# Kernel tuning notes

Measured on AMD Instinct MI355X. Metric: run time of the kernel, lower is better.

The kernel has to match this reference:

```python
import jax, jax.numpy as jnp
import numpy as np

B, N, E = 2, 2048, 1024
H = 16
NE = 16                                  # num experts
TOPN = 2
CAP = max(4, int(N * 1.25 / NE))         # expert capacity = 160 (train, cf=1.25)
HFF = int(E * 4 * 2 / 3)                 # 2730, Expert_alt hidden
EPS = 1e-9
BLOCK = 64                               # spatial block size for block-causal mask


def setup_inputs():
    key = jax.random.key(0)
    ks = jax.random.split(key, 16)
    def nrm(k, shape, s=0.02):
        return jax.random.normal(k, shape, dtype=jnp.float32) * s
    # block-causal mask (tril over time blocks, repeat_interleave spatially); True = masked
    blk = np.tril(np.ones((N // BLOCK, N // BLOCK)))
    blk = np.repeat(np.repeat(blk, BLOCK, axis=0), BLOCK, axis=1)
    attn_mask = jnp.asarray(~blk.astype(bool))
    return dict(
        x=jax.random.normal(ks[0], (B, N, E), jnp.float32),
        attn_mask=attn_mask,
        in_proj_w=nrm(ks[1], (3 * E, E)),
        in_proj_b=jnp.zeros((3 * E,), jnp.float32),
        out_proj_w=nrm(ks[2], (E, E)),
        out_proj_b=jnp.zeros((E,), jnp.float32),
        rms_gamma=jnp.ones((E,), jnp.float32),
        gate_w=nrm(ks[3], (NE, E)),
        ln_g=jnp.ones((NE, E), jnp.float32),
        ln_b=jnp.zeros((NE, E), jnp.float32),
        w1=nrm(ks[4], (NE, HFF, E)),
        b1=jnp.zeros((NE, HFF), jnp.float32),
        w2=nrm(ks[5], (NE, E, HFF)),
        b2=jnp.zeros((NE, E), jnp.float32),
        route_unif=jax.random.uniform(ks[6], (TOPN, B, N), jnp.float32),
    )


def _layernorm(t, g, b, eps=1e-5):
    mu = t.mean(-1, keepdims=True)
    var = ((t - mu) ** 2).mean(-1, keepdims=True)
    return (t - mu) * jax.lax.rsqrt(var + eps) * g + b


def _forward(x, attn_mask, in_proj_w, in_proj_b, out_proj_w, out_proj_b,
             rms_gamma, gate_w, ln_g, ln_b, w1, b1, w2, b2, route_unif):
    dh = E // H
    # ---- multi-head self-attention (torch nn.MultiheadAttention math) ----
    qkv = x @ in_proj_w.T + in_proj_b                       # (B,N,3E)
    q, k, v = jnp.split(qkv, 3, axis=-1)
    to_heads = lambda t: t.reshape(B, N, H, dh).transpose(0, 2, 1, 3)
    q, k, v = to_heads(q), to_heads(k), to_heads(v)
    scores = jnp.einsum('bhqd,bhkd->bhqk', q, k) / jnp.sqrt(jnp.float32(dh))
    scores = jnp.where(attn_mask[None, None], -jnp.inf, scores)
    attn = jax.nn.softmax(scores, axis=-1)
    o = jnp.einsum('bhqk,bhkd->bhqd', attn, v).transpose(0, 2, 1, 3).reshape(B, N, E)
    o = o @ out_proj_w.T + out_proj_b
    y = o + x                                               # residual around MHA

    # ---- SparseMoEBlock: RMSNorm prenorm -> MoE -> residual ----
    residual = y
    nrm = y / jnp.clip(jnp.linalg.norm(y, axis=-1, keepdims=True), 1e-12)
    moe_in = nrm * jnp.sqrt(jnp.float32(E)) * rms_gamma

    # ---- top-2 gating (st-moe TopNGating, training mode) ----
    logits = moe_in @ gate_w.T                              # (B,N,NE)
    raw_gates = jax.nn.softmax(logits, axis=-1)
    gates_v, gate_idx = jax.lax.top_k(raw_gates, TOPN)      # (B,N,2)
    gates = jnp.moveaxis(gates_v, -1, 0)                    # (2,B,N)
    gate_idx = jnp.moveaxis(gate_idx, -1, 0)
    one_hot_idx = jax.nn.one_hot(gate_idx, NE, dtype=jnp.float32)  # (2,B,N,NE)
    mask = one_hot_idx
    mask_1 = mask[0]
    denom = jnp.clip(gates.sum(0, keepdims=True), EPS)
    gates = gates / denom
    threshold = jnp.array([EPS, 0.2], jnp.float32)[:, None, None]
    should_route = route_unif < gates / jnp.clip(threshold, EPS)
    should_route = should_route.at[0].set(True)             # always route to top-1
    mask = mask * should_route[..., None].astype(jnp.float32)
    mask_cumsum = jnp.cumsum(mask, axis=-2) - mask          # exclusive cumsum over N

    positions, masks_k = [], []
    prev = jnp.zeros((B, 1, NE), jnp.float32)
    capf = jnp.float32(CAP)
    for n_ in range(TOPN):
        pos = (mask_cumsum[n_] + prev) * mask[n_]           # (B,N,NE)
        mk = mask[n_] * (pos < capf).astype(jnp.float32)    # drop over-capacity
        prev = prev + mk.sum(axis=-2, keepdims=True)
        positions.append(pos.sum(-1))                       # (B,N)
        masks_k.append(mk)
    positions = jnp.stack(positions)                        # (2,B,N)
    mask = jnp.stack(masks_k)
    mask_flat = mask.sum(-1)                                # (2,B,N)
    gates = gates * mask_flat

    pos_oh = jax.nn.one_hot(positions.astype(jnp.int32), CAP, dtype=jnp.float32)  # (2,B,N,CAP)
    combine = jnp.einsum('kbn,kbn,kbne,kbnc->bnec', gates, mask_flat, one_hot_idx, pos_oh)
    dispatch_hard = (combine > 0).astype(jnp.float32)
    dispatch = dispatch_hard + combine - jax.lax.stop_gradient(combine)  # straight-through

    # ---- aux losses ----
    density_1 = mask_1.mean(-2)                             # (B,NE)
    density_proxy = raw_gates.mean(-2)
    balance_loss = (density_proxy * density_1).mean() * jnp.float32(NE ** 2)
    router_z_loss = jnp.mean(jax.nn.logsumexp(logits, axis=-1) ** 2)

    # ---- dispatch -> experts -> combine ----
    expert_inputs = jnp.einsum('bnd,bnec->ebcd', moe_in, dispatch)  # (NE,B,CAP,E)

    def expert_fn(g, bl, W1, B1, W2, B2, xin):
        h = _layernorm(xin, g, bl)
        h = h @ W1.T + B1
        h = jnp.where(h >= 0, h, 0.01 * h)                  # LeakyReLU(0.01)
        return h @ W2.T + B2

    expert_out = jax.vmap(expert_fn)(ln_g, ln_b, w1, b1, w2, b2, expert_inputs)
    moe_out = jnp.einsum('bnec,ebcd->bnd', combine, expert_out)

    out = moe_out + residual
    total_aux = balance_loss * 0.01 + router_z_loss * 0.001
    return out, total_aux, balance_loss, router_z_loss


def reference(x, attn_mask, in_proj_w, in_proj_b, out_proj_w, out_proj_b,
              rms_gamma, gate_w, ln_g, ln_b, w1, b1, w2, b2, route_unif):
    return _forward(x, attn_mask, in_proj_w, in_proj_b, out_proj_w, out_proj_b,
                    rms_gamma, gate_w, ln_g, ln_b, w1, b1, w2, b2, route_unif)
```

## Files before the change

kernel.cpp:

```cpp
#include <hip/hip_runtime.h>
#include <hip/hip_bf16.h>
#include <cstdint>

#define NSEQ  2048
#define BSZ   2
#define NTOK  4096
#define EDIM  1024
#define NEXP  16
#define CAPC  160
#define HFF_R 2730
#define HFF_P 2752

typedef __bf16 bf16_t;
typedef __bf16 bf16x8 __attribute__((ext_vector_type(8)));
typedef __bf16 bf16x4 __attribute__((ext_vector_type(4)));
typedef float  f32x4  __attribute__((ext_vector_type(4)));
typedef unsigned int uint32;

__device__ inline bf16x8 zero8() {
    bf16x8 v;
#pragma unroll
    for (int i = 0; i < 8; i++) v[i] = (bf16_t)0.f;
    return v;
}
__device__ inline bf16x8 pack8(float4 a, float4 b) {
    bf16x8 v;
    v[0]=(bf16_t)a.x; v[1]=(bf16_t)a.y; v[2]=(bf16_t)a.z; v[3]=(bf16_t)a.w;
    v[4]=(bf16_t)b.x; v[5]=(bf16_t)b.y; v[6]=(bf16_t)b.z; v[7]=(bf16_t)b.w;
    return v;
}
struct hl_t { bf16_t h, l; };
__device__ inline hl_t split1(float f) {
    hl_t r;
    r.h = (bf16_t)f;
    r.l = (bf16_t)(f - (float)r.h);
    return r;
}

__global__ __launch_bounds__(256) void split_kernel(const float* __restrict__ src,
                                                    bf16_t* __restrict__ hi,
                                                    bf16_t* __restrict__ lo, int n)
{
    int i = (blockIdx.x * 256 + threadIdx.x) * 4;
    if (i >= n) return;
    float4 v = *(const float4*)(src + i);
    hl_t a = split1(v.x), b = split1(v.y), c = split1(v.z), d = split1(v.w);
    bf16x4 h, l;
    h[0] = a.h; h[1] = b.h; h[2] = c.h; h[3] = d.h;
    l[0] = a.l; l[1] = b.l; l[2] = c.l; l[3] = d.l;
    *(bf16x4*)(hi + i) = h;
    *(bf16x4*)(lo + i) = l;
}

template <int EPI, int C_SPLIT>
__global__ __launch_bounds__(256) void gemm_ps(
    const bf16_t* __restrict__ Ah_, const bf16_t* __restrict__ Al_,
    const bf16_t* __restrict__ Bh_, const bf16_t* __restrict__ Bl_,
    const float* __restrict__ bias, const float* __restrict__ resid,
    bf16_t* __restrict__ Chi, bf16_t* __restrict__ Clo, float* __restrict__ Cf,
    int M, int N, int K, int scale_cut, float scale_val)
{
    __shared__ __align__(16) bf16_t Ah[128 * 40], Al[128 * 40];
    __shared__ __align__(16) bf16_t Bh[128 * 40], Bl[128 * 40];
    const int t = threadIdx.x;
    const int m0 = blockIdx.y * 128, n0 = blockIdx.x * 128;
    const int lane = t & 63, l15 = lane & 15, lg = lane >> 4;
    const int wid = t >> 6, wm = wid >> 1, wn = wid & 1;
    const int srow = t >> 1, skc = (t & 1) * 16;

    f32x4 acc[4][4];
    const f32x4 zf = {0.f, 0.f, 0.f, 0.f};
#pragma unroll
    for (int i = 0; i < 4; i++)
#pragma unroll
        for (int j = 0; j < 4; j++) acc[i][j] = zf;

    bf16x8 sah0, sah1, sal0, sal1, sbh0, sbh1, sbl0, sbl1;
    auto LOADAB = [&](int k0) {
        long aoff = (long)(m0 + srow) * K + k0 + skc;
        sah0 = *(const bf16x8*)(Ah_ + aoff); sah1 = *(const bf16x8*)(Ah_ + aoff + 8);
        sal0 = *(const bf16x8*)(Al_ + aoff); sal1 = *(const bf16x8*)(Al_ + aoff + 8);
        long boff = (long)(n0 + srow) * K + k0 + skc;
        sbh0 = *(const bf16x8*)(Bh_ + boff); sbh1 = *(const bf16x8*)(Bh_ + boff + 8);
        sbl0 = *(const bf16x8*)(Bl_ + boff); sbl1 = *(const bf16x8*)(Bl_ + boff + 8);
    };
    auto WRITEAB = [&]() {
        *(bf16x8*)&Ah[srow * 40 + skc] = sah0; *(bf16x8*)&Ah[srow * 40 + skc + 8] = sah1;
        *(bf16x8*)&Al[srow * 40 + skc] = sal0; *(bf16x8*)&Al[srow * 40 + skc + 8] = sal1;
        *(bf16x8*)&Bh[srow * 40 + skc] = sbh0; *(bf16x8*)&Bh[srow * 40 + skc + 8] = sbh1;
        *(bf16x8*)&Bl[srow * 40 + skc] = sbl0; *(bf16x8*)&Bl[srow * 40 + skc + 8] = sbl1;
    };

    LOADAB(0);
    for (int k0 = 0; k0 < K; k0 += 32) {
        WRITEAB();
        __syncthreads();
        if (k0 + 32 < K) LOADAB(k0 + 32);
        bf16x8 amh[4], aml[4], bnh[4], bnl[4];
#pragma unroll
        for (int i = 0; i < 4; i++) {
            int base = (wm * 64 + i * 16 + l15) * 40 + lg * 8;
            amh[i] = *(const bf16x8*)&Ah[base];
            aml[i] = *(const bf16x8*)&Al[base];
        }
#pragma unroll
        for (int j = 0; j < 4; j++) {
            int base = (wn * 64 + j * 16 + l15) * 40 + lg * 8;
            bnh[j] = *(const bf16x8*)&Bh[base];
            bnl[j] = *(const bf16x8*)&Bl[base];
        }
        __builtin_amdgcn_s_setprio(1);
#pragma unroll
        for (int i = 0; i < 4; i++)
#pragma unroll
            for (int j = 0; j < 4; j++) {
                acc[i][j] = __builtin_amdgcn_mfma_f32_16x16x32_bf16(amh[i], bnh[j], acc[i][j], 0, 0, 0);
                acc[i][j] = __builtin_amdgcn_mfma_f32_16x16x32_bf16(amh[i], bnl[j], acc[i][j], 0, 0, 0);
                acc[i][j] = __builtin_amdgcn_mfma_f32_16x16x32_bf16(aml[i], bnh[j], acc[i][j], 0, 0, 0);
            }
        __builtin_amdgcn_s_setprio(0);
        __syncthreads();
    }

#pragma unroll
    for (int i = 0; i < 4; i++) {
        int mgb = m0 + wm * 64 + i * 16 + lg * 4;
#pragma unroll
        for (int j = 0; j < 4; j++) {
            int ng = n0 + wn * 64 + j * 16 + l15;
            float bval = bias[ng];
#pragma unroll
            for (int r = 0; r < 4; r++) {
                int mg = mgb + r;
                float val = acc[i][j][r] + bval;
                if (scale_cut > 0 && ng < scale_cut) val *= scale_val;
                if (EPI == 2) val += resid[(long)mg * N + ng];
                long idx = (long)mg * N + ng;
                if (C_SPLIT) {
                    bf16_t hi = (bf16_t)val;
                    Chi[idx] = hi;
                    Clo[idx] = (bf16_t)(val - (float)hi);
                } else {
                    Cf[idx] = val;
                }
            }
        }
    }
}

template <int EPI, int C_BF16>
__global__ __launch_bounds__(256) void gemm_ffn(
    const bf16_t* __restrict__ Av, const float* __restrict__ Bw,
    const float* __restrict__ bias, void* __restrict__ Cv,
    int N, int Nwr, int KA, int KB,
    long sAe, long sBe, long sBiasE, long sCe, int ldc)
{
    __shared__ __align__(16) bf16_t Alds[320 * 72];
    __shared__ __align__(16) bf16_t Blds[64 * 72];
    const int id = blockIdx.x;
    const int e = id & 15, nt = id >> 4;
    const int n0 = nt * 64;
    const int t = threadIdx.x;
    const int lane = t & 63, l15 = lane & 15, lg = lane >> 4;
    const int wid = t >> 6, wm = wid >> 1, wn = wid & 1;
    const int srow = t >> 2, scol = (t & 3) * 16;

    f32x4 acc[10][2];
    const f32x4 zf = {0.f, 0.f, 0.f, 0.f};
#pragma unroll
    for (int i = 0; i < 10; i++)
#pragma unroll
        for (int j = 0; j < 2; j++) acc[i][j] = zf;

    bf16x8 sa[5][2];
    float4 sb0, sb1, sb2, sb3;
    const float4 zf4 = {0.f, 0.f, 0.f, 0.f};
    auto LOADA = [&](int k0) {
        const bf16_t* abase = Av + (long)e * sAe + k0 + scol;
#pragma unroll
        for (int p = 0; p < 5; p++) {
            const bf16_t* ap = abase + (long)(srow + 64 * p) * KA;
            sa[p][0] = *(const bf16x8*)ap;
            sa[p][1] = *(const bf16x8*)(ap + 8);
        }
    };
    auto LOADB = [&](int k0) {
        int ng = n0 + srow;
        if (ng < N) {
            const float* bp = Bw + (long)e * sBe + (long)ng * KB + k0 + scol;
            if (k0 + 64 <= KB) {
                sb0 = *(const float4*)bp;       sb1 = *(const float4*)(bp + 4);
                sb2 = *(const float4*)(bp + 8); sb3 = *(const float4*)(bp + 12);
            } else {
                float v[16];
#pragma unroll
                for (int i = 0; i < 16; i++) {
                    int kk = k0 + scol + i;
                    v[i] = (kk < KB) ? bp[i] : 0.f;
                }
                sb0 = *(float4*)&v[0];  sb1 = *(float4*)&v[4];
                sb2 = *(float4*)&v[8];  sb3 = *(float4*)&v[12];
            }
        } else {
            sb0 = zf4; sb1 = zf4; sb2 = zf4; sb3 = zf4;
        }
    };
    auto WRITEAB = [&]() {
#pragma unroll
        for (int p = 0; p < 5; p++) {
            *(bf16x8*)&Alds[(srow + 64 * p) * 72 + scol]     = sa[p][0];
            *(bf16x8*)&Alds[(srow + 64 * p) * 72 + scol + 8] = sa[p][1];
        }
        *(bf16x8*)&Blds[srow * 72 + scol]     = pack8(sb0, sb1);
        *(bf16x8*)&Blds[srow * 72 + scol + 8] = pack8(sb2, sb3);
    };

    LOADA(0); LOADB(0);
    for (int k0 = 0; k0 < KA; k0 += 64) {
        WRITEAB();
        __syncthreads();
        if (k0 + 64 < KA) { LOADA(k0 + 64); LOADB(k0 + 64); }
#pragma unroll
        for (int ks = 0; ks < 2; ks++) {
            bf16x8 bn[2];
#pragma unroll
            for (int j = 0; j < 2; j++)
                bn[j] = *(const bf16x8*)&Blds[(wn * 32 + j * 16 + l15) * 72 + ks * 32 + lg * 8];
            bf16x8 am[10];
#pragma unroll
            for (int i = 0; i < 10; i++)
                am[i] = *(const bf16x8*)&Alds[(wm * 160 + i * 16 + l15) * 72 + ks * 32 + lg * 8];
            __builtin_amdgcn_s_setprio(1);
#pragma unroll
            for (int i = 0; i < 10; i++)
#pragma unroll
                for (int j = 0; j < 2; j++)
                    acc[i][j] = __builtin_amdgcn_mfma_f32_16x16x32_bf16(am[i], bn[j], acc[i][j], 0, 0, 0);
            __builtin_amdgcn_s_setprio(0);
        }
        __syncthreads();
    }

    const float* biasp = bias + (long)e * sBiasE;
#pragma unroll
    for (int i = 0; i < 10; i++) {
        int mgb = wm * 160 + i * 16 + lg * 4;
#pragma unroll
        for (int j = 0; j < 2; j++) {
            int ng = n0 + wn * 32 + j * 16 + l15;
            if (ng < Nwr) {
                float bval = (ng < N) ? biasp[ng] : 0.f;
#pragma unroll
                for (int r = 0; r < 4; r++) {
                    int mg = mgb + r;
                    float val = acc[i][j][r] + bval;
                    if (EPI == 1) val = (val >= 0.f) ? val : 0.01f * val;
                    if (ng >= N) val = 0.f;
                    long cidx = (long)e * sCe + (long)mg * ldc + ng;
                    if (C_BF16) ((bf16_t*)Cv)[cidx] = (bf16_t)val;
                    else        ((float*)Cv)[cidx] = val;
                }
            }
        }
    }
}

__global__ __launch_bounds__(256) void attn_split(const bf16_t* __restrict__ qh,
                                                  const bf16_t* __restrict__ ql,
                                                  bf16_t* __restrict__ oh,
                                                  bf16_t* __restrict__ ol)
{
    __shared__ __align__(16) bf16_t KhS[64 * 72], KlS[64 * 72];
    __shared__ __align__(16) bf16_t VhS[64 * 72], VlS[64 * 72];
    __shared__ __align__(16) bf16_t PhS[4][2][16 * 72], PlS[4][2][16 * 72];

    const int id = blockIdx.x;
    const int x  = id & 7;
    const int s  = id >> 3;
    const int b  = s >> 5;
    const int s5 = s & 31;
    const int qraw = s5 & 15;
    const int h  = x + 8 * (s5 >> 4);
    const int qt = b ? (15 - qraw) : qraw;
    const int nkb = 2 * qt + 2;

    const int t = threadIdx.x, wid = t >> 6, lane = t & 63, l15 = lane & 15, lg = lane >> 4;
    const int krow = t >> 2, kdc = (t & 3) * 16;
    const int vk = t & 63, vdg = (t >> 6) * 16;
    const long kvb = (long)(b * NSEQ) * 3072 + 1024 + h * 64;
    const f32x4 zf = {0.f, 0.f, 0.f, 0.f};

    const long qo0 = (long)(b * NSEQ + qt * 128 + wid * 16 + l15) * 3072 + h * 64 + lg * 8;
    const long qo1 = qo0 + (long)64 * 3072;
    bf16x8 q0h0 = *(const bf16x8*)(qh + qo0), q0h1 = *(const bf16x8*)(qh + qo0 + 32);
    bf16x8 q0l0 = *(const bf16x8*)(ql + qo0), q0l1 = *(const bf16x8*)(ql + qo0 + 32);
    bf16x8 q1h0 = *(const bf16x8*)(qh + qo1), q1h1 = *(const bf16x8*)(qh + qo1 + 32);
    bf16x8 q1l0 = *(const bf16x8*)(ql + qo1), q1l1 = *(const bf16x8*)(ql + qo1 + 32);

    f32x4 O0[4], O1[4];
    float m0r[4], l0r[4], m1r[4], l1r[4];
#pragma unroll
    for (int r = 0; r < 4; r++) {
        O0[r] = zf; O1[r] = zf;
        m0r[r] = -1e30f; l0r[r] = 0.f; m1r[r] = -1e30f; l1r[r] = 0.f;
    }

    bf16x8 skh0, skh1, skl0, skl1, svh0, svh1, svl0, svl1;
    auto LOADKV = [&](int kb) {
        long ko = kvb + (long)(kb * 64 + krow) * 3072 + kdc;
        skh0 = *(const bf16x8*)(qh + ko); skh1 = *(const bf16x8*)(qh + ko + 8);
        skl0 = *(const bf16x8*)(ql + ko); skl1 = *(const bf16x8*)(ql + ko + 8);
        long vo = kvb + 1024 + (long)(kb * 64 + vk) * 3072 + vdg;
        svh0 = *(const bf16x8*)(qh + vo); svh1 = *(const bf16x8*)(qh + vo + 8);
        svl0 = *(const bf16x8*)(ql + vo); svl1 = *(const bf16x8*)(ql + vo + 8);
    };
    auto WRITEKV = [&]() {
        *(bf16x8*)&KhS[krow * 72 + kdc]     = skh0;
        *(bf16x8*)&KhS[krow * 72 + kdc + 8] = skh1;
        *(bf16x8*)&KlS[krow * 72 + kdc]     = skl0;
        *(bf16x8*)&KlS[krow * 72 + kdc + 8] = skl1;
#pragma unroll
        for (int i = 0; i < 8; i++) {
            VhS[(vdg + i) * 72 + vk]     = svh0[i];
            VhS[(vdg + 8 + i) * 72 + vk] = svh1[i];
            VlS[(vdg + i) * 72 + vk]     = svl0[i];
            VlS[(vdg + 8 + i) * 72 + vk] = svl1[i];
        }
    };

    LOADKV(0);
    for (int kb = 0; kb < nkb; kb++) {
        __syncthreads();
        WRITEKV();
        __syncthreads();
        if (kb + 1 < nkb) LOADKV(kb + 1);
        const bool g0a = (kb < nkb - 1);
        f32x4 s0[4], s1[4];
        __builtin_amdgcn_s_setprio(1);
#pragma unroll
        for (int ks = 0; ks < 4; ks++) {
            int base = (ks * 16 + l15) * 72 + lg * 8;
            bf16x8 kh0 = *(const bf16x8*)&KhS[base];
            bf16x8 kh1 = *(const bf16x8*)&KhS[base + 32];
            bf16x8 kl0 = *(const bf16x8*)&KlS[base];
            bf16x8 kl1 = *(const bf16x8*)&KlS[base + 32];
            f32x4 a = zf;
            a = __builtin_amdgcn_mfma_f32_16x16x32_bf16(q1h0, kh0, a, 0, 0, 0);
            a = __builtin_amdgcn_mfma_f32_16x16x32_bf16(q1h1, kh1, a, 0, 0, 0);
            a = __builtin_amdgcn_mfma_f32_16x16x32_bf16(q1h0, kl0, a, 0, 0, 0);
            a = __builtin_amdgcn_mfma_f32_16x16x32_bf16(q1h1, kl1, a, 0, 0, 0);
            a = __builtin_amdgcn_mfma_f32_16x16x32_bf16(q1l0, kh0, a, 0, 0, 0);
            a = __builtin_amdgcn_mfma_f32_16x16x32_bf16(q1l1, kh1, a, 0, 0, 0);
            s1[ks] = a;
            f32x4 c = zf;
            if (g0a) {
                c = __builtin_amdgcn_mfma_f32_16x16x32_bf16(q0h0, kh0, c, 0, 0, 0);
                c = __builtin_amdgcn_mfma_f32_16x16x32_bf16(q0h1, kh1, c, 0, 0, 0);
                c = __builtin_amdgcn_mfma_f32_16x16x32_bf16(q0h0, kl0, c, 0, 0, 0);
                c = __builtin_amdgcn_mfma_f32_16x16x32_bf16(q0h1, kl1, c, 0, 0, 0);
                c = __builtin_amdgcn_mfma_f32_16x16x32_bf16(q0l0, kh0, c, 0, 0, 0);
                c = __builtin_amdgcn_mfma_f32_16x16x32_bf16(q0l1, kh1, c, 0, 0, 0);
            }
            s0[ks] = c;
        }
        __builtin_amdgcn_s_setprio(0);
        {
            float alpha[4];
#pragma unroll
            for (int r = 0; r < 4; r++) {
                float mt = fmaxf(fmaxf(s1[0][r], s1[1][r]), fmaxf(s1[2][r], s1[3][r]));
#pragma unroll
                for (int m = 1; m < 16; m <<= 1) mt = fmaxf(mt, __shfl_xor(mt, m));
                float mn = fmaxf(m1r[r], mt);
                alpha[r] = __expf(m1r[r] - mn);
                m1r[r] = mn;
            }
            float ladd[4] = {0.f, 0.f, 0.f, 0.f};
#pragma unroll
            for (int ks = 0; ks < 4; ks++)
#pragma unroll
                for (int r = 0; r < 4; r++) {
                    float p = __expf(s1[ks][r] - m1r[r]);
                    s1[ks][r] = p;
                    ladd[r] += p;
                }
#pragma unroll
            for (int r = 0; r < 4; r++) {
#pragma unroll
                for (int m = 1; m < 16; m <<= 1) ladd[r] += __shfl_xor(ladd[r], m);
                l1r[r] = l1r[r] * alpha[r] + ladd[r];
            }
#pragma unroll
            for (int sb = 0; sb < 4; sb++)
#pragma unroll
                for (int r = 0; r < 4; r++) O1[sb][r] *= alpha[r];
            bf16_t* pwh = &PhS[wid][1][0];
            bf16_t* pwl = &PlS[wid][1][0];
#pragma unroll
            for (int ks = 0; ks < 4; ks++)
#pragma unroll
                for (int r = 0; r < 4; r++) {
                    hl_t pv = split1(s1[ks][r]);
                    pwh[(lg * 4 + r) * 72 + ks * 16 + l15] = pv.h;
                    pwl[(lg * 4 + r) * 72 + ks * 16 + l15] = pv.l;
                }
        }
        if (g0a) {
            float alpha[4];
#pragma unroll
            for (int r = 0; r < 4; r++) {
                float mt = fmaxf(fmaxf(s0[0][r], s0[1][r]), fmaxf(s0[2][r], s0[3][r]));
#pragma unroll
                for (int m = 1; m < 16; m <<= 1) mt = fmaxf(mt, __shfl_xor(mt, m));
                float mn = fmaxf(m0r[r], mt);
                alpha[r] = __expf(m0r[r] - mn);
                m0r[r] = mn;
            }
            float ladd[4] = {0.f, 0.f, 0.f, 0.f};
#pragma unroll
            for (int ks = 0; ks < 4; ks++)
#pragma unroll
                for (int r = 0; r < 4; r++) {
                    float p = __expf(s0[ks][r] - m0r[r]);
                    s0[ks][r] = p;
                    ladd[r] += p;
                }
#pragma unroll
            for (int r = 0; r < 4; r++) {
#pragma unroll
                for (int m = 1; m < 16; m <<= 1) ladd[r] += __shfl_xor(ladd[r], m);
                l0r[r] = l0r[r] * alpha[r] + ladd[r];
            }
#pragma unroll
            for (int sb = 0; sb < 4; sb++)
#pragma unroll
                for (int r = 0; r < 4; r++) O0[sb][r] *= alpha[r];
            bf16_t* pwh = &PhS[wid][0][0];
            bf16_t* pwl = &PlS[wid][0][0];
#pragma unroll
            for (int ks = 0; ks < 4; ks++)
#pragma unroll
                for (int r = 0; r < 4; r++) {
                    hl_t pv = split1(s0[ks][r]);
                    pwh[(lg * 4 + r) * 72 + ks * 16 + l15] = pv.h;
                    pwl[(lg * 4 + r) * 72 + ks * 16 + l15] = pv.l;
                }
        }
        __builtin_amdgcn_s_setprio(1);
#pragma unroll
        for (int kst = 0; kst < 2; kst++) {
            bf16x8 pf1h = *(const bf16x8*)&PhS[wid][1][l15 * 72 + kst * 32 + lg * 8];
            bf16x8 pf1l = *(const bf16x8*)&PlS[wid][1][l15 * 72 + kst * 32 + lg * 8];
            bf16x8 pf0h, pf0l;
            if (g0a) {
                pf0h = *(const bf16x8*)&PhS[wid][0][l15 * 72 + kst * 32 + lg * 8];
                pf0l = *(const bf16x8*)&PlS[wid][0][l15 * 72 + kst * 32 + lg * 8];
            }
#pragma unroll
            for (int sb = 0; sb < 4; sb++) {
                int base = (sb * 16 + l15) * 72 + kst * 32 + lg * 8;
                bf16x8 vfh = *(const bf16x8*)&VhS[base];
                bf16x8 vfl = *(const bf16x8*)&VlS[base];
                O1[sb] = __builtin_amdgcn_mfma_f32_16x16x32_bf16(pf1h, vfh, O1[sb], 0, 0, 0);
                O1[sb] = __builtin_amdgcn_mfma_f32_16x16x32_bf16(pf1h, vfl, O1[sb], 0, 0, 0);
                O1[sb] = __builtin_amdgcn_mfma_f32_16x16x32_bf16(pf1l, vfh, O1[sb], 0, 0, 0);
                if (g0a) {
                    O0[sb] = __builtin_amdgcn_mfma_f32_16x16x32_bf16(pf0h, vfh, O0[sb], 0, 0, 0);
                    O0[sb] = __builtin_amdgcn_mfma_f32_16x16x32_bf16(pf0h, vfl, O0[sb], 0, 0, 0);
                    O0[sb] = __builtin_amdgcn_mfma_f32_16x16x32_bf16(pf0l, vfh, O0[sb], 0, 0, 0);
                }
            }
        }
        __builtin_amdgcn_s_setprio(0);
    }
#pragma unroll
    for (int sb = 0; sb < 4; sb++)
#pragma unroll
        for (int r = 0; r < 4; r++) {
            int qg0 = qt * 128 + wid * 16 + lg * 4 + r;
            int col = h * 64 + sb * 16 + l15;
            long i0 = (long)(b * NSEQ + qg0) * 1024 + col;
            long i1 = (long)(b * NSEQ + qg0 + 64) * 1024 + col;
            hl_t v0 = split1(O0[sb][r] / l0r[r]);
            hl_t v1 = split1(O1[sb][r] / l1r[r]);
            oh[i0] = v0.h; ol[i0] = v0.l;
            oh[i1] = v1.h; ol[i1] = v1.l;
        }
}

__global__ __launch_bounds__(256) void rmsnorm_kernel(const float* __restrict__ y,
                                                      const float* __restrict__ gamma,
                                                      float* __restrict__ moe)
{
    long base = (long)blockIdx.x * 1024;
    float4 v = ((const float4*)(y + base))[threadIdx.x];
    float ss = v.x * v.x + v.y * v.y + v.z * v.z + v.w * v.w;
#pragma unroll
    for (int m = 32; m; m >>= 1) ss += __shfl_xor(ss, m);
    __shared__ float ls[4];
    if ((threadIdx.x & 63) == 0) ls[threadIdx.x >> 6] = ss;
    __syncthreads();
    float tot = ls[0] + ls[1] + ls[2] + ls[3];
    float sc = 32.0f / fmaxf(sqrtf(tot), 1e-12f);
    float4 g = ((const float4*)gamma)[threadIdx.x];
    float4 ov;
    ov.x = v.x * sc * g.x; ov.y = v.y * sc * g.y; ov.z = v.z * sc * g.z; ov.w = v.w * sc * g.w;
    ((float4*)(moe + base))[threadIdx.x] = ov;
}

__global__ __launch_bounds__(256) void gating_kernel(
    const float* __restrict__ moe, const float* __restrict__ gw,
    const float* __restrict__ runif, uint32* __restrict__ tokpack,
    float* __restrict__ tokg, float* __restrict__ acc)
{
    const int wid = threadIdx.x >> 6, lane = threadIdx.x & 63;
    const int tk = blockIdx.x * 4 + wid;
    const int b = tk >> 11, n = tk & 2047;
    float xv[16];
    const float4* xr4 = (const float4*)(moe + (long)tk * 1024 + lane * 16);
#pragma unroll
    for (int i = 0; i < 4; i++) {
        float4 v = xr4[i];
        xv[4 * i] = v.x; xv[4 * i + 1] = v.y; xv[4 * i + 2] = v.z; xv[4 * i + 3] = v.w;
    }
    float logit[16];
#pragma unroll
    for (int e = 0; e < 16; e++) {
        const float4* wr4 = (const float4*)(gw + e * 1024 + lane * 16);
        float p = 0.f;
#pragma unroll
        for (int i = 0; i < 4; i++) {
            float4 w = wr4[i];
            p = fmaf(xv[4 * i], w.x, p);     p = fmaf(xv[4 * i + 1], w.y, p);
            p = fmaf(xv[4 * i + 2], w.z, p); p = fmaf(xv[4 * i + 3], w.w, p);
        }
#pragma unroll
        for (int m = 1; m < 64; m <<= 1) p += __shfl_xor(p, m);
        logit[e] = p;
    }
    int e0 = 0; float t0 = logit[0];
#pragma unroll
    for (int e = 1; e < 16; e++) if (logit[e] > t0) { t0 = logit[e]; e0 = e; }
    int e1 = (e0 == 0) ? 1 : 0; float t1 = logit[e1];
#pragma unroll
    for (int e = 0; e < 16; e++) if (e != e0 && logit[e] > t1) { t1 = logit[e]; e1 = e; }
    float g0n = 1.f / (1.f + __expf(t1 - t0));
    float g1n = 1.f / (1.f + __expf(t0 - t1));
    int sr1 = (runif[(long)(BSZ + b) * NSEQ + n] < g1n / 0.2f) ? 1 : 0;
    float mx = t0, sum = 0.f, raw[16];
#pragma unroll
    for (int e = 0; e < 16; e++) { raw[e] = __expf(logit[e] - mx); sum += raw[e]; }
    float inv = 1.f / sum;
    float lse = mx + __logf(sum);
    if (lane == 0) {
        tokpack[tk] = (uint32)e0 | ((uint32)e1 << 4) | ((uint32)sr1 << 8);
        tokg[2 * tk] = g0n; tokg[2 * tk + 1] = g1n;
        atomicAdd(&acc[32 + b * 16 + e0], 1.0f);
        atomicAdd(&acc[64], lse * lse);
    }
    if (lane < 16) atomicAdd(&acc[b * 16 + lane], raw[lane] * inv);
}

__global__ __launch_bounds__(512) void scan_kernel(const uint32* __restrict__ tokpack,
                                                   uint32* __restrict__ r0,
                                                   uint32* __restrict__ r1,
                                                   int* __restrict__ prev)
{
    const int b = blockIdx.x, t = threadIdx.x;
    const int wv = t >> 6, lane = t & 63;
    uint32 toks[4];
    *(uint4*)toks = ((const uint4*)(tokpack + b * NSEQ))[t];

    uint32 c0[8], c1[8];
#pragma unroll
    for (int j = 0; j < 8; j++) { c0[j] = 0u; c1[j] = 0u; }
#pragma unroll
    for (int i = 0; i < 4; i++) {
        uint32 p = toks[i];
        uint32 e0 = p & 15, e1 = (p >> 4) & 15, sr1 = (p >> 8) & 1;
        uint32 inc0 = 1u << ((e0 & 1) * 16);
        uint32 inc1 = sr1 << ((e1 & 1) * 16);
#pragma unroll
        for (int j = 0; j < 8; j++) {
            c0[j] += ((e0 >> 1) == (uint32)j) ? inc0 : 0u;
            c1[j] += ((e1 >> 1) == (uint32)j) ? inc1 : 0u;
        }
    }
    uint32 i0[8], i1[8];
#pragma unroll
    for (int j = 0; j < 8; j++) { i0[j] = c0[j]; i1[j] = c1[j]; }
#pragma unroll
    for (int off = 1; off < 64; off <<= 1) {
#pragma unroll
        for (int j = 0; j < 8; j++) {
            uint32 u0 = __shfl_up(i0[j], off);
            uint32 u1 = __shfl_up(i1[j], off);
            if (lane >= off) { i0[j] += u0; i1[j] += u1; }
        }
    }
    __shared__ uint32 wsum0[8][8], wsum1[8][8];
    if (lane == 63) {
#pragma unroll
        for (int j = 0; j < 8; j++) { wsum0[wv][j] = i0[j]; wsum1[wv][j] = i1[j]; }
    }
    __syncthreads();
    uint32 b0[8], b1[8];
#pragma unroll
    for (int j = 0; j < 8; j++) {
        uint32 s0 = 0u, s1 = 0u;
#pragma unroll
        for (int w = 0; w < 8; w++) {
            s0 += (w < wv) ? wsum0[w][j] : 0u;
            s1 += (w < wv) ? wsum1[w][j] : 0u;
        }
        b0[j] = s0 + i0[j] - c0[j];
        b1[j] = s1 + i1[j] - c1[j];
    }
    if (t == 0) {
#pragma unroll
        for (int j = 0; j < 8; j++) {
            uint32 tot = 0u;
#pragma unroll
            for (int w = 0; w < 8; w++) tot += wsum0[w][j];
            int tlo = (int)(tot & 0xffffu), thi = (int)(tot >> 16);
            prev[b * 16 + 2 * j]     = tlo < CAPC ? tlo : CAPC;
            prev[b * 16 + 2 * j + 1] = thi < CAPC ? thi : CAPC;
        }
    }
    uint32* rr0 = r0 + b * NSEQ + t * 4;
    uint32* rr1 = r1 + b * NSEQ + t * 4;
#pragma unroll
    for (int i = 0; i < 4; i++) {
        uint32 p = toks[i];
        uint32 e0 = p & 15, e1 = (p >> 4) & 15, sr1 = (p >> 8) & 1;
        uint32 sh0 = (e0 & 1) * 16, sh1 = (e1 & 1) * 16;
        uint32 w0 = 0u, w1 = 0u;
#pragma unroll
        for (int j = 0; j < 8; j++) {
            w0 += ((e0 >> 1) == (uint32)j) ? b0[j] : 0u;
            w1 += ((e1 >> 1) == (uint32)j) ? b1[j] : 0u;
        }
        uint32 s0 = (w0 >> sh0) & 0xffffu;
        uint32 s1v = (w1 >> sh1) & 0xffffu;
        uint32 kept = (s0 < CAPC) ? 1u : 0u;
        rr0[i] = e0 | (kept << 4) | (s0 << 5);
        rr1[i] = e1 | (sr1 << 4) | (s1v << 5);
        uint32 inc0 = 1u << sh0;
        uint32 inc1 = sr1 << sh1;
#pragma unroll
        for (int j = 0; j < 8; j++) {
            b0[j] += ((e0 >> 1) == (uint32)j) ? inc0 : 0u;
            b1[j] += ((e1 >> 1) == (uint32)j) ? inc1 : 0u;
        }
    }
}

__global__ __launch_bounds__(256) void gather_kernel(
    const float* __restrict__ moe, const uint32* __restrict__ r0,
    const uint32* __restrict__ r1, const int* __restrict__ prev,
    float* __restrict__ ein)
{
    int tk = blockIdx.x, b = tk >> 11;
    float4 v = ((const float4*)(moe + (long)tk * 1024))[threadIdx.x];
    uint32 a = r0[tk];
    if ((a >> 4) & 1) {
        long row = ((long)(a & 15) * 2 + b) * CAPC + (int)(a >> 5);
        ((float4*)(ein + row * 1024))[threadIdx.x] = v;
    }
    uint32 c = r1[tk];
    {
        int e = c & 15, sr1 = (c >> 4) & 1;
        int slot = (int)(c >> 5) + prev[b * 16 + e];
        if (sr1 && slot < CAPC) {
            long row = ((long)e * 2 + b) * CAPC + slot;
            ((float4*)(ein + row * 1024))[threadIdx.x] = v;
        }
    }
}

__global__ __launch_bounds__(256) void expert_ln_kernel(
    const float* __restrict__ ein, const float* __restrict__ g,
    const float* __restrict__ bb, bf16_t* __restrict__ eout)
{
    int row = blockIdx.x, e = row / (BSZ * CAPC);
    long base = (long)row * 1024;
    float4 v = ((const float4*)(ein + base))[threadIdx.x];
    float s = v.x + v.y + v.z + v.w;
    float ss = v.x * v.x + v.y * v.y + v.z * v.z + v.w * v.w;
#pragma unroll
    for (int m = 32; m; m >>= 1) { s += __shfl_xor(s, m); ss += __shfl_xor(ss, m); }
    __shared__ float l1[4], l2[4];
    if ((threadIdx.x & 63) == 0) { l1[threadIdx.x >> 6] = s; l2[threadIdx.x >> 6] = ss; }
    __syncthreads();
    float st = l1[0] + l1[1] + l1[2] + l1[3];
    float sst = l2[0] + l2[1] + l2[2] + l2[3];
    float mu = st * (1.f / 1024.f);
    float var = sst * (1.f / 1024.f) - mu * mu;
    float rstd = rsqrtf(var + 1e-5f);
    int d = threadIdx.x * 4;
    float4 gg = *(const float4*)(g + e * 1024 + d);
    float4 bv = *(const float4*)(bb + e * 1024 + d);
    bf16x4 ov;
    ov[0] = (bf16_t)((v.x - mu) * rstd * gg.x + bv.x);
    ov[1] = (bf16_t)((v.y - mu) * rstd * gg.y + bv.y);
    ov[2] = (bf16_t)((v.z - mu) * rstd * gg.z + bv.z);
    ov[3] = (bf16_t)((v.w - mu) * rstd * gg.w + bv.w);
    *(bf16x4*)(eout + base + d) = ov;
}

__global__ __launch_bounds__(256) void combine_kernel(
    const float* __restrict__ y, const float* __restrict__ eout,
    const uint32* __restrict__ r0, const uint32* __restrict__ r1,
    const float* __restrict__ tokg, const int* __restrict__ prev,
    float* __restrict__ out)
{
    int tk = blockIdx.x, b = tk >> 11;
    uint32 a = r0[tk], c = r1[tk];
    int k0f = (a >> 4) & 1;
    float w0 = k0f ? tokg[2 * tk] : 0.f;
    long row0 = ((long)(a & 15) * 2 + b) * CAPC + (int)(a >> 5);
    int e1 = c & 15;
    int slot1 = (int)(c >> 5) + prev[b * 16 + e1];
    int k1f = (((c >> 4) & 1) && slot1 < CAPC) ? 1 : 0;
    float w1 = k1f ? tokg[2 * tk + 1] : 0.f;
    long row1 = ((long)e1 * 2 + b) * CAPC + slot1;
    int i = threadIdx.x;
    float4 vy = ((const float4*)(y + (long)tk * 1024))[i];
    float4 a0 = {0.f, 0.f, 0.f, 0.f}, a1 = {0.f, 0.f, 0.f, 0.f};
    if (k0f) a0 = ((const float4*)(eout + row0 * 1024))[i];
    if (k1f) a1 = ((const float4*)(eout + row1 * 1024))[i];
    float4 ov;
    ov.x = vy.x + w0 * a0.x + w1 * a1.x;
    ov.y = vy.y + w0 * a0.y + w1 * a1.y;
    ov.z = vy.z + w0 * a0.z + w1 * a1.z;
    ov.w = vy.w + w0 * a0.w + w1 * a1.w;
    ((float4*)(out + (long)tk * 1024))[i] = ov;
}

__global__ void zero_acc_kernel(float* acc)
{
    if (threadIdx.x < 65) acc[threadIdx.x] = 0.f;
}

__global__ void finalize_kernel(const float* __restrict__ acc, float* __restrict__ tail)
{
    int t = threadIdx.x;
    float v = (t < 32) ? acc[t] * acc[32 + t] : 0.f;
#pragma unroll
    for (int m = 1; m < 64; m <<= 1) v += __shfl_xor(v, m);
    if (t == 0) {
        float bal = v * (8.0f / (2048.f * 2048.f));
        float z = acc[64] / 4096.f;
        tail[0] = 0.01f * bal + 0.001f * z;
        tail[1] = bal;
        tail[2] = z;
    }
}

extern "C" void kernel_launch(void* const* d_in, const int* in_sizes, int n_in,
                              void* d_out, int out_size, void* d_ws, size_t ws_size,
                              hipStream_t stream)
{
    (void)in_sizes; (void)n_in; (void)out_size; (void)ws_size;
    const float* x     = (const float*)d_in[0];
    const float* in_w  = (const float*)d_in[2];
    const float* in_b  = (const float*)d_in[3];
    const float* out_w = (const float*)d_in[4];
    const float* out_b = (const float*)d_in[5];
    const float* rg    = (const float*)d_in[6];
    const float* gw    = (const float*)d_in[7];
    const float* lng   = (const float*)d_in[8];
    const float* lnb   = (const float*)d_in[9];
    const float* w1    = (const float*)d_in[10];
    const float* b1    = (const float*)d_in[11];
    const float* w2    = (const float*)d_in[12];
    const float* b2    = (const float*)d_in[13];
    const float* runif = (const float*)d_in[14];
    float* out = (float*)d_out;

    size_t off = 0;
    char* wsb = (char*)d_ws;
    auto take = [&](size_t bytes) -> char* {
        char* p = wsb + off;
        off += (bytes + 255) & ~(size_t)255;
        return p;
    };
    bf16_t* qkvh = (bf16_t*)take((size_t)NTOK * 3072 * 2);
    bf16_t* qkvl = (bf16_t*)take((size_t)NTOK * 3072 * 2);
    bf16_t* oh   = (bf16_t*)take((size_t)NTOK * 1024 * 2);
    bf16_t* ol   = (bf16_t*)take((size_t)NTOK * 1024 * 2);
    float*  ybuf = (float*)take((size_t)NTOK * 1024 * 4);
    float*  moe  = (float*)take((size_t)NTOK * 1024 * 4);
    bf16_t* eln  = (bf16_t*)take((size_t)NEXP * BSZ * CAPC * 1024 * 2);
    bf16_t* hbuf = (bf16_t*)take((size_t)NEXP * BSZ * CAPC * HFF_P * 2);
    bf16_t* owh  = (bf16_t*)take((size_t)1024 * 1024 * 2);
    bf16_t* owl  = (bf16_t*)take((size_t)1024 * 1024 * 2);
    uint32* tokpack = (uint32*)take(NTOK * 4);
    float*  tokg = (float*)take(NTOK * 8);
    uint32* r0   = (uint32*)take(NTOK * 4);
    uint32* r1   = (uint32*)take(NTOK * 4);
    int*    prev = (int*)take(128);
    float*  acc  = (float*)take(1024);
    float*  ein   = (float*)qkvl;
    float*  eoutv = (float*)qkvh;
    bf16_t* xh    = eln;
    bf16_t* xl    = xh + (size_t)NTOK * 1024;
    bf16_t* iwh   = xl + (size_t)NTOK * 1024;
    bf16_t* iwl   = iwh + (size_t)3072 * 1024;

    zero_acc_kernel<<<1, 128, 0, stream>>>(acc);

    split_kernel<<<dim3(NTOK * 1024 / 1024), 256, 0, stream>>>(x, xh, xl, NTOK * 1024);
    split_kernel<<<dim3(3072 * 1024 / 1024), 256, 0, stream>>>(in_w, iwh, iwl, 3072 * 1024);
    split_kernel<<<dim3(1024 * 1024 / 1024), 256, 0, stream>>>(out_w, owh, owl, 1024 * 1024);

    gemm_ps<0, 1><<<dim3(24, 32), 256, 0, stream>>>(
        xh, xl, iwh, iwl, in_b, nullptr, qkvh, qkvl, nullptr,
        NTOK, 3072, 1024, 1024, 0.125f);

    attn_split<<<dim3(512), 256, 0, stream>>>(qkvh, qkvl, oh, ol);

    gemm_ps<2, 0><<<dim3(8, 32), 256, 0, stream>>>(
        oh, ol, owh, owl, out_b, x, nullptr, nullptr, ybuf,
        NTOK, 1024, 1024, 0, 1.0f);

    rmsnorm_kernel<<<NTOK, 256, 0, stream>>>(ybuf, rg, moe);
    gating_kernel<<<NTOK / 4, 256, 0, stream>>>(moe, gw, runif, tokpack, tokg, acc);
    scan_kernel<<<dim3(BSZ), 512, 0, stream>>>(tokpack, r0, r1, prev);
    gather_kernel<<<NTOK, 256, 0, stream>>>(moe, r0, r1, prev, ein);
    expert_ln_kernel<<<NEXP * BSZ * CAPC, 256, 0, stream>>>(ein, lng, lnb, eln);

    gemm_ffn<1, 1><<<dim3(43 * 16), 256, 0, stream>>>(
        eln, w1, b1, hbuf, HFF_R, HFF_P, 1024, 1024,
        (long)320 * 1024, (long)HFF_R * 1024, HFF_R, (long)320 * HFF_P, HFF_P);

    gemm_ffn<0, 0><<<dim3(16 * 16), 256, 0, stream>>>(
        hbuf, w2, b2, eoutv, 1024, 1024, HFF_P, HFF_R,
        (long)320 * HFF_P, (long)1024 * HFF_R, 1024, (long)320 * 1024, 1024);

    combine_kernel<<<NTOK, 256, 0, stream>>>(ybuf, eoutv, r0, r1, tokg, prev, out);
    finalize_kernel<<<1, 64, 0, stream>>>(acc, out + (size_t)NTOK * 1024);
}
```

Baseline: 584.9 us.

## Split attention query tiles across eight waves and fuse expert gather with LayerNorm

The attention kernel now launches 512 threads per block. Each of eight waves owns one 16-row query strip, where before four waves each carried two strips. This halves per-wave register state (Q fragments, O accumulators, softmax stats) and doubles the waves available to hide latency. The cost is that the waves on the diagonal-masked half sit idle on the last key block. Separately, the expert gather and expert LayerNorm are merged into one kernel that normalizes each token once and writes bf16 rows directly. This removes the fp32 intermediate expert-input buffer round trip and one kernel launch.

```diff
diff --git a/kernel.cpp b/kernel.cpp
--- a/kernel.cpp
+++ b/kernel.cpp
@@ -265,14 +265,14 @@
     }
 }
 
-__global__ __launch_bounds__(256) void attn_split(const bf16_t* __restrict__ qh,
+__global__ __launch_bounds__(512) void attn_split(const bf16_t* __restrict__ qh,
                                                   const bf16_t* __restrict__ ql,
                                                   bf16_t* __restrict__ oh,
                                                   bf16_t* __restrict__ ol)
 {
     __shared__ __align__(16) bf16_t KhS[64 * 72], KlS[64 * 72];
     __shared__ __align__(16) bf16_t VhS[64 * 72], VlS[64 * 72];
-    __shared__ __align__(16) bf16_t PhS[4][2][16 * 72], PlS[4][2][16 * 72];
+    __shared__ __align__(16) bf16_t PhS[8][16 * 72], PlS[8][16 * 72];
 
     const int id = blockIdx.x;
     const int x  = id & 7;
@@ -285,46 +285,36 @@
     const int nkb = 2 * qt + 2;
 
     const int t = threadIdx.x, wid = t >> 6, lane = t & 63, l15 = lane & 15, lg = lane >> 4;
-    const int krow = t >> 2, kdc = (t & 3) * 16;
-    const int vk = t & 63, vdg = (t >> 6) * 16;
+    const int krow = t >> 3, kdc = (t & 7) * 8;
+    const int vk = t & 63, vdg = (t >> 6) * 8;
     const long kvb = (long)(b * NSEQ) * 3072 + 1024 + h * 64;
     const f32x4 zf = {0.f, 0.f, 0.f, 0.f};
 
-    const long qo0 = (long)(b * NSEQ + qt * 128 + wid * 16 + l15) * 3072 + h * 64 + lg * 8;
-    const long qo1 = qo0 + (long)64 * 3072;
-    bf16x8 q0h0 = *(const bf16x8*)(qh + qo0), q0h1 = *(const bf16x8*)(qh + qo0 + 32);
-    bf16x8 q0l0 = *(const bf16x8*)(ql + qo0), q0l1 = *(const bf16x8*)(ql + qo0 + 32);
-    bf16x8 q1h0 = *(const bf16x8*)(qh + qo1), q1h1 = *(const bf16x8*)(qh + qo1 + 32);
-    bf16x8 q1l0 = *(const bf16x8*)(ql + qo1), q1l1 = *(const bf16x8*)(ql + qo1 + 32);
-
-    f32x4 O0[4], O1[4];
-    float m0r[4], l0r[4], m1r[4], l1r[4];
-#pragma unroll
-    for (int r = 0; r < 4; r++) {
-        O0[r] = zf; O1[r] = zf;
-        m0r[r] = -1e30f; l0r[r] = 0.f; m1r[r] = -1e30f; l1r[r] = 0.f;
-    }
-
-    bf16x8 skh0, skh1, skl0, skl1, svh0, svh1, svl0, svl1;
+    const long qo = (long)(b * NSEQ + qt * 128 + wid * 16 + l15) * 3072 + h * 64 + lg * 8;
+    bf16x8 qh0 = *(const bf16x8*)(qh + qo), qh1 = *(const bf16x8*)(qh + qo + 32);
+    bf16x8 ql0 = *(const bf16x8*)(ql + qo), ql1 = *(const bf16x8*)(ql + qo + 32);
+
+    f32x4 O[4];
+    float mr[4], lr[4];
+#pragma unroll
+    for (int r = 0; r < 4; r++) { O[r] = zf; mr[r] = -1e30f; lr[r] = 0.f; }
+
+    bf16x8 skh, skl, svh, svl;
     auto LOADKV = [&](int kb) {
         long ko = kvb + (long)(kb * 64 + krow) * 3072 + kdc;
-        skh0 = *(const bf16x8*)(qh + ko); skh1 = *(const bf16x8*)(qh + ko + 8);
-        skl0 = *(const bf16x8*)(ql + ko); skl1 = *(const bf16x8*)(ql + ko + 8);
+        skh = *(const bf16x8*)(qh + ko);
+        skl = *(const bf16x8*)(ql + ko);
         long vo = kvb + 1024 + (long)(kb * 64 + vk) * 3072 + vdg;
-        svh0 = *(const bf16x8*)(qh + vo); svh1 = *(const bf16x8*)(qh + vo + 8);
-        svl0 = *(const bf16x8*)(ql + vo); svl1 = *(const bf16x8*)(ql + vo + 8);
+        svh = *(const bf16x8*)(qh + vo);
+        svl = *(const bf16x8*)(ql + vo);
     };
     auto WRITEKV = [&]() {
-        *(bf16x8*)&KhS[krow * 72 + kdc]     = skh0;
-        *(bf16x8*)&KhS[krow * 72 + kdc + 8] = skh1;
-        *(bf16x8*)&KlS[krow * 72 + kdc]     = skl0;
-        *(bf16x8*)&KlS[krow * 72 + kdc + 8] = skl1;
+        *(bf16x8*)&KhS[krow * 72 + kdc] = skh;
+        *(bf16x8*)&KlS[krow * 72 + kdc] = skl;
 #pragma unroll
         for (int i = 0; i < 8; i++) {
-            VhS[(vdg + i) * 72 + vk]     = svh0[i];
-            VhS[(vdg + 8 + i) * 72 + vk] = svh1[i];
-            VlS[(vdg + i) * 72 + vk]     = svl0[i];
-            VlS[(vdg + 8 + i) * 72 + vk] = svl1[i];
+            VhS[(vdg + i) * 72 + vk] = svh[i];
+            VlS[(vdg + i) * 72 + vk] = svl[i];
         }
     };
 
@@ -334,157 +324,93 @@
         WRITEKV();
         __syncthreads();
         if (kb + 1 < nkb) LOADKV(kb + 1);
-        const bool g0a = (kb < nkb - 1);
-        f32x4 s0[4], s1[4];
-        __builtin_amdgcn_s_setprio(1);
-#pragma unroll
-        for (int ks = 0; ks < 4; ks++) {
-            int base = (ks * 16 + l15) * 72 + lg * 8;
-            bf16x8 kh0 = *(const bf16x8*)&KhS[base];
-            bf16x8 kh1 = *(const bf16x8*)&KhS[base + 32];
-            bf16x8 kl0 = *(const bf16x8*)&KlS[base];
-            bf16x8 kl1 = *(const bf16x8*)&KlS[base + 32];
-            f32x4 a = zf;
-            a = __builtin_amdgcn_mfma_f32_16x16x32_bf16(q1h0, kh0, a, 0, 0, 0);
-            a = __builtin_amdgcn_mfma_f32_16x16x32_bf16(q1h1, kh1, a, 0, 0, 0);
-            a = __builtin_amdgcn_mfma_f32_16x16x32_bf16(q1h0, kl0, a, 0, 0, 0);
-            a = __builtin_amdgcn_mfma_f32_16x16x32_bf16(q1h1, kl1, a, 0, 0, 0);
-            a = __builtin_amdgcn_mfma_f32_16x16x32_bf16(q1l0, kh0, a, 0, 0, 0);
-            a = __builtin_amdgcn_mfma_f32_16x16x32_bf16(q1l1, kh1, a, 0, 0, 0);
-            s1[ks] = a;
-            f32x4 c = zf;
-            if (g0a) {
-                c = __builtin_amdgcn_mfma_f32_16x16x32_bf16(q0h0, kh0, c, 0, 0, 0);
-                c = __builtin_amdgcn_mfma_f32_16x16x32_bf16(q0h1, kh1, c, 0, 0, 0);
-                c = __builtin_amdgcn_mfma_f32_16x16x32_bf16(q0h0, kl0, c, 0, 0, 0);
-                c = __builtin_amdgcn_mfma_f32_16x16x32_bf16(q0h1, kl1, c, 0, 0, 0);
-                c = __builtin_amdgcn_mfma_f32_16x16x32_bf16(q0l0, kh0, c, 0, 0, 0);
-                c = __builtin_amdgcn_mfma_f32_16x16x32_bf16(q0l1, kh1, c, 0, 0, 0);
+        const bool act = (wid >= 4) || (kb < nkb - 1);
+        if (act) {
+            f32x4 sv[4];
+            __builtin_amdgcn_s_setprio(1);
+#pragma unroll
+            for (int ks = 0; ks < 4; ks++) {
+                int base = (ks * 16 + l15) * 72 + lg * 8;
+                bf16x8 kh0 = *(const bf16x8*)&KhS[base];
+                bf16x8 kh1 = *(const bf16x8*)&KhS[base + 32];
+                bf16x8 kl0 = *(const bf16x8*)&KlS[base];
+                bf16x8 kl1 = *(const bf16x8*)&KlS[base + 32];
+                f32x4 a = zf;
+                a = __builtin_amdgcn_mfma_f32_16x16x32_bf16(qh0, kh0, a, 0, 0, 0);
+                a = __builtin_amdgcn_mfma_f32_16x16x32_bf16(qh1, kh1, a, 0, 0, 0);
+                a = __builtin_amdgcn_mfma_f32_16x16x32_bf16(qh0, kl0, a, 0, 0, 0);
+                a = __builtin_amdgcn_mfma_f32_16x16x32_bf16(qh1, kl1, a, 0, 0, 0);
+                a = __builtin_amdgcn_mfma_f32_16x16x32_bf16(ql0, kh0, a, 0, 0, 0);
+                a = __builtin_amdgcn_mfma_f32_16x16x32_bf16(ql1, kh1, a, 0, 0, 0);
+                sv[ks] = a;
             }
-            s0[ks] = c;
-        }
-        __builtin_amdgcn_s_setprio(0);
-        {
+            __builtin_amdgcn_s_setprio(0);
             float alpha[4];
 #pragma unroll
             for (int r = 0; r < 4; r++) {
-                float mt = fmaxf(fmaxf(s1[0][r], s1[1][r]), fmaxf(s1[2][r], s1[3][r]));
+                float mt = fmaxf(fmaxf(sv[0][r], sv[1][r]), fmaxf(sv[2][r], sv[3][r]));
 #pragma unroll
                 for (int m = 1; m < 16; m <<= 1) mt = fmaxf(mt, __shfl_xor(mt, m));
-                float mn = fmaxf(m1r[r], mt);
-                alpha[r] = __expf(m1r[r] - mn);
-                m1r[r] = mn;
+                float mn = fmaxf(mr[r], mt);
+                alpha[r] = __expf(mr[r] - mn);
+                mr[r] = mn;
             }
             float ladd[4] = {0.f, 0.f, 0.f, 0.f};
 #pragma unroll
             for (int ks = 0; ks < 4; ks++)
 #pragma unroll
                 for (int r = 0; r < 4; r++) {
-                    float p = __expf(s1[ks][r] - m1r[r]);
-                    s1[ks][r] = p;
+                    float p = __expf(sv[ks][r] - mr[r]);
+                    sv[ks][r] = p;
                     ladd[r] += p;
                 }
 #pragma unroll
             for (int r = 0; r < 4; r++) {
 #pragma unroll
                 for (int m = 1; m < 16; m <<= 1) ladd[r] += __shfl_xor(ladd[r], m);
-                l1r[r] = l1r[r] * alpha[r] + ladd[r];
+                lr[r] = lr[r] * alpha[r] + ladd[r];
             }
 #pragma unroll
             for (int sb = 0; sb < 4; sb++)
 #pragma unroll
-                for (int r = 0; r < 4; r++) O1[sb][r] *= alpha[r];
-            bf16_t* pwh = &PhS[wid][1][0];
-            bf16_t* pwl = &PlS[wid][1][0];
+                for (int r = 0; r < 4; r++) O[sb][r] *= alpha[r];
+            bf16_t* pwh = &PhS[wid][0];
+            bf16_t* pwl = &PlS[wid][0];
 #pragma unroll
             for (int ks = 0; ks < 4; ks++)
 #pragma unroll
                 for (int r = 0; r < 4; r++) {
-                    hl_t pv = split1(s1[ks][r]);
+                    hl_t pv = split1(sv[ks][r]);
                     pwh[(lg * 4 + r) * 72 + ks * 16 + l15] = pv.h;
                     pwl[(lg * 4 + r) * 72 + ks * 16 + l15] = pv.l;
                 }
-        }
-        if (g0a) {
-            float alpha[4];
-#pragma unroll
-            for (int r = 0; r < 4; r++) {
-                float mt = fmaxf(fmaxf(s0[0][r], s0[1][r]), fmaxf(s0[2][r], s0[3][r]));
-#pragma unroll
-                for (int m = 1; m < 16; m <<= 1) mt = fmaxf(mt, __shfl_xor(mt, m));
-                float mn = fmaxf(m0r[r], mt);
-                alpha[r] = __expf(m0r[r] - mn);
-                m0r[r] = mn;
-            }
-            float ladd[4] = {0.f, 0.f, 0.f, 0.f};
-#pragma unroll
-            for (int ks = 0; ks < 4; ks++)
-#pragma unroll
-                for (int r = 0; r < 4; r++) {
-                    float p = __expf(s0[ks][r] - m0r[r]);
-                    s0[ks][r] = p;
-                    ladd[r] += p;
-                }
-#pragma unroll
-            for (int r = 0; r < 4; r++) {
-#pragma unroll
-                for (int m = 1; m < 16; m <<= 1) ladd[r] += __shfl_xor(ladd[r], m);
-                l0r[r] = l0r[r] * alpha[r] + ladd[r];
-            }
-#pragma unroll
-            for (int sb = 0; sb < 4; sb++)
-#pragma unroll
-                for (int r = 0; r < 4; r++) O0[sb][r] *= alpha[r];
-            bf16_t* pwh = &PhS[wid][0][0];
-            bf16_t* pwl = &PlS[wid][0][0];
-#pragma unroll
-            for (int ks = 0; ks < 4; ks++)
-#pragma unroll
-                for (int r = 0; r < 4; r++) {
-                    hl_t pv = split1(s0[ks][r]);
-                    pwh[(lg * 4 + r) * 72 + ks * 16 + l15] = pv.h;
-                    pwl[(lg * 4 + r) * 72 + ks * 16 + l15] = pv.l;
-                }
-        }
-        __builtin_amdgcn_s_setprio(1);
-#pragma unroll
-        for (int kst = 0; kst < 2; kst++) {
-            bf16x8 pf1h = *(const bf16x8*)&PhS[wid][1][l15 * 72 + kst * 32 + lg * 8];
-            bf16x8 pf1l = *(const bf16x8*)&PlS[wid][1][l15 * 72 + kst * 32 + lg * 8];
-            bf16x8 pf0h, pf0l;
-            if (g0a) {
-                pf0h = *(const bf16x8*)&PhS[wid][0][l15 * 72 + kst * 32 + lg * 8];
-                pf0l = *(const bf16x8*)&PlS[wid][0][l15 * 72 + kst * 32 + lg * 8];
-            }
-#pragma unroll
-            for (int sb = 0; sb < 4; sb++) {
-                int base = (sb * 16 + l15) * 72 + kst * 32 + lg * 8;
-                bf16x8 vfh = *(const bf16x8*)&VhS[base];
-                bf16x8 vfl = *(const bf16x8*)&VlS[base];
-                O1[sb] = __builtin_amdgcn_mfma_f32_16x16x32_bf16(pf1h, vfh, O1[sb], 0, 0, 0);
-                O1[sb] = __builtin_amdgcn_mfma_f32_16x16x32_bf16(pf1h, vfl, O1[sb], 0, 0, 0);
-                O1[sb] = __builtin_amdgcn_mfma_f32_16x16x32_bf16(pf1l, vfh, O1[sb], 0, 0, 0);
-                if (g0a) {
-                    O0[sb] = __builtin_amdgcn_mfma_f32_16x16x32_bf16(pf0h, vfh, O0[sb], 0, 0, 0);
-                    O0[sb] = __builtin_amdgcn_mfma_f32_16x16x32_bf16(pf0h, vfl, O0[sb], 0, 0, 0);
-                    O0[sb] = __builtin_amdgcn_mfma_f32_16x16x32_bf16(pf0l, vfh, O0[sb], 0, 0, 0);
+            __builtin_amdgcn_s_setprio(1);
+#pragma unroll
+            for (int kst = 0; kst < 2; kst++) {
+                bf16x8 pfh = *(const bf16x8*)&pwh[l15 * 72 + kst * 32 + lg * 8];
+                bf16x8 pfl = *(const bf16x8*)&pwl[l15 * 72 + kst * 32 + lg * 8];
+#pragma unroll
+                for (int sb = 0; sb < 4; sb++) {
+                    int base = (sb * 16 + l15) * 72 + kst * 32 + lg * 8;
+                    bf16x8 vfh = *(const bf16x8*)&VhS[base];
+                    bf16x8 vfl = *(const bf16x8*)&VlS[base];
+                    O[sb] = __builtin_amdgcn_mfma_f32_16x16x32_bf16(pfh, vfh, O[sb], 0, 0, 0);
+                    O[sb] = __builtin_amdgcn_mfma_f32_16x16x32_bf16(pfh, vfl, O[sb], 0, 0, 0);
+                    O[sb] = __builtin_amdgcn_mfma_f32_16x16x32_bf16(pfl, vfh, O[sb], 0, 0, 0);
                 }
             }
-        }
-        __builtin_amdgcn_s_setprio(0);
+            __builtin_amdgcn_s_setprio(0);
+        }
     }
 #pragma unroll
     for (int sb = 0; sb < 4; sb++)
 #pragma unroll
         for (int r = 0; r < 4; r++) {
-            int qg0 = qt * 128 + wid * 16 + lg * 4 + r;
+            int qg = qt * 128 + wid * 16 + lg * 4 + r;
             int col = h * 64 + sb * 16 + l15;
-            long i0 = (long)(b * NSEQ + qg0) * 1024 + col;
-            long i1 = (long)(b * NSEQ + qg0 + 64) * 1024 + col;
-            hl_t v0 = split1(O0[sb][r] / l0r[r]);
-            hl_t v1 = split1(O1[sb][r] / l1r[r]);
+            long i0 = (long)(b * NSEQ + qg) * 1024 + col;
+            hl_t v0 = split1(O[sb][r] / lr[r]);
             oh[i0] = v0.h; ol[i0] = v0.l;
-            oh[i1] = v1.h; ol[i1] = v1.l;
         }
 }
 
@@ -655,36 +581,14 @@
     }
 }
 
-__global__ __launch_bounds__(256) void gather_kernel(
+__global__ __launch_bounds__(256) void gather_ln_kernel(
     const float* __restrict__ moe, const uint32* __restrict__ r0,
     const uint32* __restrict__ r1, const int* __restrict__ prev,
-    float* __restrict__ ein)
+    const float* __restrict__ g, const float* __restrict__ bb,
+    bf16_t* __restrict__ eln)
 {
     int tk = blockIdx.x, b = tk >> 11;
     float4 v = ((const float4*)(moe + (long)tk * 1024))[threadIdx.x];
-    uint32 a = r0[tk];
-    if ((a >> 4) & 1) {
-        long row = ((long)(a & 15) * 2 + b) * CAPC + (int)(a >> 5);
-        ((float4*)(ein + row * 1024))[threadIdx.x] = v;
-    }
-    uint32 c = r1[tk];
-    {
-        int e = c & 15, sr1 = (c >> 4) & 1;
-        int slot = (int)(c >> 5) + prev[b * 16 + e];
-        if (sr1 && slot < CAPC) {
-            long row = ((long)e * 2 + b) * CAPC + slot;
-            ((float4*)(ein + row * 1024))[threadIdx.x] = v;
-        }
-    }
-}
-
-__global__ __launch_bounds__(256) void expert_ln_kernel(
-    const float* __restrict__ ein, const float* __restrict__ g,
-    const float* __restrict__ bb, bf16_t* __restrict__ eout)
-{
-    int row = blockIdx.x, e = row / (BSZ * CAPC);
-    long base = (long)row * 1024;
-    float4 v = ((const float4*)(ein + base))[threadIdx.x];
     float s = v.x + v.y + v.z + v.w;
     float ss = v.x * v.x + v.y * v.y + v.z * v.z + v.w * v.w;
 #pragma unroll
@@ -698,14 +602,38 @@
     float var = sst * (1.f / 1024.f) - mu * mu;
     float rstd = rsqrtf(var + 1e-5f);
     int d = threadIdx.x * 4;
-    float4 gg = *(const float4*)(g + e * 1024 + d);
-    float4 bv = *(const float4*)(bb + e * 1024 + d);
-    bf16x4 ov;
-    ov[0] = (bf16_t)((v.x - mu) * rstd * gg.x + bv.x);
-    ov[1] = (bf16_t)((v.y - mu) * rstd * gg.y + bv.y);
-    ov[2] = (bf16_t)((v.z - mu) * rstd * gg.z + bv.z);
-    ov[3] = (bf16_t)((v.w - mu) * rstd * gg.w + bv.w);
-    *(bf16x4*)(eout + base + d) = ov;
+    float nx = (v.x - mu) * rstd, ny = (v.y - mu) * rstd;
+    float nz = (v.z - mu) * rstd, nw = (v.w - mu) * rstd;
+
+    uint32 a = r0[tk];
+    if ((a >> 4) & 1) {
+        int e = a & 15;
+        long row = ((long)e * 2 + b) * CAPC + (int)(a >> 5);
+        float4 gg = *(const float4*)(g + e * 1024 + d);
+        float4 bv = *(const float4*)(bb + e * 1024 + d);
+        bf16x4 ov;
+        ov[0] = (bf16_t)(nx * gg.x + bv.x);
+        ov[1] = (bf16_t)(ny * gg.y + bv.y);
+        ov[2] = (bf16_t)(nz * gg.z + bv.z);
+        ov[3] = (bf16_t)(nw * gg.w + bv.w);
+        *(bf16x4*)(eln + row * 1024 + d) = ov;
+    }
+    uint32 c = r1[tk];
+    {
+        int e = c & 15, sr1 = (c >> 4) & 1;
+        int slot = (int)(c >> 5) + prev[b * 16 + e];
+        if (sr1 && slot < CAPC) {
+            long row = ((long)e * 2 + b) * CAPC + slot;
+            float4 gg = *(const float4*)(g + e * 1024 + d);
+            float4 bv = *(const float4*)(bb + e * 1024 + d);
+            bf16x4 ov;
+            ov[0] = (bf16_t)(nx * gg.x + bv.x);
+            ov[1] = (bf16_t)(ny * gg.y + bv.y);
+            ov[2] = (bf16_t)(nz * gg.z + bv.z);
+            ov[3] = (bf16_t)(nw * gg.w + bv.w);
+            *(bf16x4*)(eln + row * 1024 + d) = ov;
+        }
+    }
 }
 
 __global__ __launch_bounds__(256) void combine_kernel(
@@ -801,7 +729,6 @@
     uint32* r1   = (uint32*)take(NTOK * 4);
     int*    prev = (int*)take(128);
     float*  acc  = (float*)take(1024);
-    float*  ein   = (float*)qkvl;
     float*  eoutv = (float*)qkvh;
     bf16_t* xh    = eln;
     bf16_t* xl    = xh + (size_t)NTOK * 1024;
@@ -818,7 +745,7 @@
         xh, xl, iwh, iwl, in_b, nullptr, qkvh, qkvl, nullptr,
         NTOK, 3072, 1024, 1024, 0.125f);
 
-    attn_split<<<dim3(512), 256, 0, stream>>>(qkvh, qkvl, oh, ol);
+    attn_split<<<dim3(512), 512, 0, stream>>>(qkvh, qkvl, oh, ol);
 
     gemm_ps<2, 0><<<dim3(8, 32), 256, 0, stream>>>(
         oh, ol, owh, owl, out_b, x, nullptr, nullptr, ybuf,
@@ -827,8 +754,7 @@
     rmsnorm_kernel<<<NTOK, 256, 0, stream>>>(ybuf, rg, moe);
     gating_kernel<<<NTOK / 4, 256, 0, stream>>>(moe, gw, runif, tokpack, tokg, acc);
     scan_kernel<<<dim3(BSZ), 512, 0, stream>>>(tokpack, r0, r1, prev);
-    gather_kernel<<<NTOK, 256, 0, stream>>>(moe, r0, r1, prev, ein);
-    expert_ln_kernel<<<NEXP * BSZ * CAPC, 256, 0, stream>>>(ein, lng, lnb, eln);
+    gather_ln_kernel<<<NTOK, 256, 0, stream>>>(moe, r0, r1, prev, lng, lnb, eln);
 
     gemm_ffn<1, 1><<<dim3(43 * 16), 256, 0, stream>>>(
         eln, w1, b1, hbuf, HFF_R, HFF_P, 1024, 1024,
```

Measured after the change: 565.2 us (median of 3 runs). 3.4% less time.
